# Optimization experiments

Measured on AMD Instinct MI355X. Metric: run time of the kernel, lower is better.

The kernel has to match this reference:

```python
import jax, jax.numpy as jnp
import numpy as np

D_MODEL = 256
N_HEADS = 8
HEAD_DIM = D_MODEL // N_HEADS


def setup_inputs() -> dict:
    key = jax.random.key(0)
    ks = jax.random.split(key, 10)
    B, L, D = 2, 2048, D_MODEL
    s = 1.0 / np.sqrt(D)
    inp = {
        "x": jax.random.normal(ks[0], (B, L, D), dtype=jnp.float32),
        "Wq": jax.random.normal(ks[1], (D, D), dtype=jnp.float32) * s,
        "bq": jnp.zeros((D,), jnp.float32),
        "Wk": jax.random.normal(ks[2], (D, D), dtype=jnp.float32) * s,
        "bk": jnp.zeros((D,), jnp.float32),
        "Wv": jax.random.normal(ks[3], (D, D), dtype=jnp.float32) * s,
        "bv": jnp.zeros((D,), jnp.float32),
        "u": jax.random.normal(ks[4], (N_HEADS, 1, 1), dtype=jnp.float32) * 0.1,
        "Wo": jax.random.normal(ks[5], (D, D), dtype=jnp.float32) * s,
        "bo": jnp.zeros((D,), jnp.float32),
    }
    return inp


def reference(x, Wq, bq, Wk, bk, Wv, bv, u, Wo, bo):
    B, L, D = x.shape
    H, hd = N_HEADS, HEAD_DIM

    def proj(W, b):  # torch Linear: x @ W.T + b -> [B,H,L,hd]
        return (x @ W.T + b).reshape(B, L, H, hd).transpose(0, 2, 1, 3)

    Q, K, V = proj(Wq, bq), proj(Wk, bk), proj(Wv, bv)

    scores = jnp.einsum("bhqd,bhkd->bhqk", Q, K) / np.sqrt(hd)
    attn_series = jax.nn.softmax(scores, axis=-1)  # [B,H,L,L]

    pos = jnp.arange(L, dtype=jnp.float32)
    dist = jnp.abs(pos[None, :] - pos[:, None])  # [L,L]
    # prior per head: exp(-d^2 / (2*(u^2+1e-6))), normalized over last dim
    prior = jnp.exp(-(dist[None] ** 2) / (2.0 * (u ** 2 + 1e-6)))  # [H,L,L]
    prior = prior / (prior.sum(axis=-1, keepdims=True) + 1e-6)

    discrepancy = jnp.abs(attn_series - prior[None]).mean(axis=(1, 2))  # [B,L]

    out = jnp.einsum("bhqk,bhkd->bhqd", attn_series, V)
    out = out.transpose(0, 2, 1, 3).reshape(B, L, D)
    out = out @ Wo.T + bo
    return out, discrepancy
```

## Files before the change

### kernel.cpp

```cpp
#include <hip/hip_runtime.h>
#include <hip/hip_bf16.h>
#include <math.h>

#define LSEQ 2048
#define DMODEL 256
#define NH 8
#define HD 32

typedef __attribute__((ext_vector_type(8))) short bf16x8;
typedef __attribute__((ext_vector_type(4))) float f32x4;

#define MFMA __builtin_amdgcn_mfma_f32_16x16x32_bf16

__device__ __forceinline__ short f2bf(float x) {
  __hip_bfloat16 h = __float2bfloat16(x);
  return __builtin_bit_cast(short, h);
}
__device__ __forceinline__ float bf2f(short s) {
  __hip_bfloat16 h = __builtin_bit_cast(__hip_bfloat16, s);
  return __bfloat162float(h);
}
__device__ __forceinline__ short bftrunc(float x) {
  return (short)(__builtin_bit_cast(unsigned int, x) >> 16);
}
__device__ __forceinline__ float fexp2(float x) {
#if __has_builtin(__builtin_amdgcn_exp2f)
  return __builtin_amdgcn_exp2f(x);
#else
  return __expf(x * 0.6931471805599453f);
#endif
}
__device__ __forceinline__ float flog2(float x) {
#if __has_builtin(__builtin_amdgcn_logf)
  return __builtin_amdgcn_logf(x);
#else
  return __logf(x) * 1.4426950408889634f;
#endif
}

__global__ __launch_bounds__(256) void aux_kernel(
    const float* __restrict__ Wq, const float* __restrict__ Wk,
    const float* __restrict__ Wv, const float* __restrict__ Wo,
    const float* __restrict__ u,
    short* __restrict__ Wh,
    short* __restrict__ Woh, short* __restrict__ Wol,
    float* __restrict__ Eb, float* __restrict__ Zb)
{
  __shared__ float Cs[LSEQ];
  __shared__ float part[256];
  const int tid = threadIdx.x;
  if (blockIdx.x < 256) {
    const int i4 = (blockIdx.x * 256 + tid) * 4;
    if (i4 < 196608) {
      int row = i4 >> 8, col = i4 & 255;
      const float* W = (row < 256) ? Wq : (row < 512) ? Wk : Wv;
      float4 v = *(const float4*)(W + (row & 255) * 256 + col);
      *(short4*)(Wh + i4) = make_short4(f2bf(v.x), f2bf(v.y), f2bf(v.z), f2bf(v.w));
    } else {
      int j = i4 - 196608;
      float4 v = *(const float4*)(Wo + j);
      short h0 = f2bf(v.x), h1 = f2bf(v.y), h2 = f2bf(v.z), h3 = f2bf(v.w);
      *(short4*)(Woh + j) = make_short4(h0, h1, h2, h3);
      *(short4*)(Wol + j) = make_short4(bftrunc(v.x - bf2f(h0)), bftrunc(v.y - bf2f(h1)),
                                        bftrunc(v.z - bf2f(h2)), bftrunc(v.w - bf2f(h3)));
    }
    return;
  }
  const int h = blockIdx.x - 256;
  const float uu = u[h];
  const float den = 2.0f * (uu * uu + 1e-6f);
  float e[8]; float run = 0.f;
  const int base = tid * 8;
#pragma unroll
  for (int j = 0; j < 8; ++j) {
    float d = (float)(base + j);
    e[j] = __expf(-(d * d) / den);
    run += e[j];
  }
  part[tid] = run;
  __syncthreads();
  for (int off = 1; off < 256; off <<= 1) {
    float v = (tid >= off) ? part[tid - off] : 0.f;
    __syncthreads();
    part[tid] += v;
    __syncthreads();
  }
  float c = part[tid] - run;
#pragma unroll
  for (int j = 0; j < 8; ++j) {
    c += e[j];
    Cs[base + j] = c;
    Eb[h * LSEQ + base + j] = e[j];
  }
  __syncthreads();
  const float E0 = Cs[0];
  for (int i = tid; i < LSEQ; i += 256) {
    float s = Cs[i] + Cs[LSEQ - 1 - i] - E0;
    Zb[h * LSEQ + i] = 1.0f / (s + 1e-6f);
  }
}

__global__ __launch_bounds__(256) void qkv_gemm(
    const float* __restrict__ x,
    const short* __restrict__ Bh,
    const float* __restrict__ bq, const float* __restrict__ bk,
    const float* __restrict__ bv,
    short* __restrict__ Qf, short* __restrict__ Kf, short* __restrict__ Vf)
{
  const int tid = threadIdx.x, w = tid >> 6, lane = tid & 63;
  const int l15 = lane & 15, q4 = lane >> 4;
  const int m0 = blockIdx.x * 64, n0 = blockIdx.y * 64;
  const int mrow = m0 + w * 16 + l15;
  f32x4 acc[4] = {{0,0,0,0},{0,0,0,0},{0,0,0,0},{0,0,0,0}};
  for (int k0 = 0; k0 < 256; k0 += 32) {
    const float* xp = &x[(size_t)mrow * 256 + k0 + q4 * 8];
    float4 a = *(const float4*)xp;
    float4 c = *(const float4*)(xp + 4);
    bf16x8 ah;
    ah[0] = f2bf(a.x); ah[1] = f2bf(a.y); ah[2] = f2bf(a.z); ah[3] = f2bf(a.w);
    ah[4] = f2bf(c.x); ah[5] = f2bf(c.y); ah[6] = f2bf(c.z); ah[7] = f2bf(c.w);
#pragma unroll
    for (int nt = 0; nt < 4; ++nt) {
      const size_t bi = (size_t)(n0 + nt * 16 + l15) * 256 + k0 + q4 * 8;
      bf16x8 bh = *(const bf16x8*)&Bh[bi];
      acc[nt] = MFMA(ah, bh, acc[nt], 0, 0, 0);
    }
  }
  const int type = n0 >> 8;
  const int n0l = n0 & 255;
  const float* bias = (type == 0) ? bq : (type == 1) ? bk : bv;
  const float qls = 0.25503489f;
#pragma unroll
  for (int nt = 0; nt < 4; ++nt) {
    const int col = n0l + nt * 16 + l15;
    const float bvv = bias[col];
    const int hh = col >> 5, dloc = col & 31;
#pragma unroll
    for (int r = 0; r < 4; ++r) {
      const int m = m0 + w * 16 + q4 * 4 + r;
      float v = acc[nt][r] + bvv;
      const int bb = m >> 11, mm = m & 2047, rr = mm & 15;
      if (type == 2) {
        const int kt128 = mm >> 7, low7 = mm & 127;
        const int wv = (low7 >> 4) & 3, ph = low7 >> 6;
        const int c = ph * 16 + rr;
        const size_t idx =
          ((((((size_t)bb * 8 + hh) * 16 + kt128) * 4 + wv) * 2 + (dloc >> 4)) * 64
           + (c >> 3) * 16 + (dloc & 15)) * 8 + (c & 7);
        Vf[idx] = f2bf(v);
      } else if (type == 0) {
        const int qblk = mm >> 5, rg = (mm >> 4) & 1;
        const size_t idx =
          (((((size_t)bb * 8 + hh) * 64 + qblk) * 2 + rg) * 64
           + (dloc >> 3) * 16 + rr) * 8 + (dloc & 7);
        Qf[idx] = f2bf(v * qls);
      } else {
        const int g = mm >> 4;
        const size_t idx =
          ((((size_t)bb * 8 + hh) * 128 + g) * 64
           + (dloc >> 3) * 16 + rr) * 8 + (dloc & 7);
        Kf[idx] = f2bf(v);
      }
    }
  }
}

__global__ __launch_bounds__(256) void out_gemm(
    const short* __restrict__ Ah, const short* __restrict__ Al,
    const short* __restrict__ Bh, const short* __restrict__ Bl,
    const float* __restrict__ bias, float* __restrict__ C)
{
  const int tid = threadIdx.x, w = tid >> 6, lane = tid & 63;
  const int l15 = lane & 15, q4 = lane >> 4;
  const int m0 = blockIdx.x * 64, n0 = blockIdx.y * 64;
  const int mrow = m0 + w * 16 + l15;
  f32x4 acc[4] = {{0,0,0,0},{0,0,0,0},{0,0,0,0},{0,0,0,0}};
  for (int k0 = 0; k0 < 256; k0 += 32) {
    bf16x8 ah = *(const bf16x8*)&Ah[(size_t)mrow * 256 + k0 + q4 * 8];
    bf16x8 al = *(const bf16x8*)&Al[(size_t)mrow * 256 + k0 + q4 * 8];
#pragma unroll
    for (int nt = 0; nt < 4; ++nt) {
      const size_t bi = (size_t)(n0 + nt * 16 + l15) * 256 + k0 + q4 * 8;
      bf16x8 bh = *(const bf16x8*)&Bh[bi];
      bf16x8 bl = *(const bf16x8*)&Bl[bi];
      acc[nt] = MFMA(ah, bh, acc[nt], 0, 0, 0);
      acc[nt] = MFMA(al, bh, acc[nt], 0, 0, 0);
      acc[nt] = MFMA(ah, bl, acc[nt], 0, 0, 0);
    }
  }
#pragma unroll
  for (int nt = 0; nt < 4; ++nt) {
    const int col = n0 + nt * 16 + l15;
    const float bvv = bias[col];
#pragma unroll
    for (int r = 0; r < 4; ++r) {
      const int m = m0 + w * 16 + q4 * 4 + r;
      C[(size_t)m * 256 + col] = acc[nt][r] + bvv;
    }
  }
}

__global__ __launch_bounds__(256, 8) void attn_kernel(
    const short* __restrict__ Qf, const short* __restrict__ Kf,
    const short* __restrict__ Vf,
    const float* __restrict__ Eb, const float* __restrict__ Zb,
    short* __restrict__ Ohb, short* __restrict__ Olb,
    short* __restrict__ Dp)
{
  __shared__ short Pt[4][16][40];
  __shared__ float Elds[192];
  __shared__ float lpart[4][16];
  __shared__ float izlds[16];

  const int tid = threadIdx.x, w = tid >> 6, lane = tid & 63;
  const int l15 = lane & 15, q4 = lane >> 4;
  const int flat = blockIdx.x + 128 * (blockIdx.y + 8 * blockIdx.z);
  const int slot = flat >> 3;
  const int g = (flat & 7) | ((slot >> 7) << 3);
  const int h = g & 7, b = g >> 3;
  const int qslot = slot & 127, q0 = qslot * 16;
  const int bh = b * NH + h;

  if (tid < 192) Elds[tid] = Eb[h * LSEQ + tid];
  if (tid < 16)  izlds[tid] = Zb[h * LSEQ + q0 + tid];

  const bf16x8* Qf8 = (const bf16x8*)Qf;
  const bf16x8* Kf8 = (const bf16x8*)Kf;
  const bf16x8* Vf8 = (const bf16x8*)Vf;

  bf16x8 qh = Qf8[((size_t)bh * 128 + qslot) * 64 + lane];
  __syncthreads();

  const size_t kfb = (size_t)bh * 128;
  const size_t vfb = (size_t)bh * 16;

  float lac[4] = {0.f, 0.f, 0.f, 0.f};
#pragma unroll 2
  for (int kt = 0; kt < LSEQ; kt += 128) {
    bf16x8 k0 = Kf8[(kfb + (kt >> 4) + w) * 64 + lane];
    bf16x8 k1 = Kf8[(kfb + (kt >> 4) + 4 + w) * 64 + lane];
    f32x4 s0 = {0.f, 0.f, 0.f, 0.f};
    s0 = MFMA(qh, k0, s0, 0, 0, 0);
    f32x4 s1 = {0.f, 0.f, 0.f, 0.f};
    s1 = MFMA(qh, k1, s1, 0, 0, 0);
#pragma unroll
    for (int r = 0; r < 4; ++r) lac[r] += fexp2(s0[r]) + fexp2(s1[r]);
  }
#pragma unroll
  for (int r = 0; r < 4; ++r) {
    float v = lac[r];
    v += __shfl_xor(v, 1); v += __shfl_xor(v, 2);
    v += __shfl_xor(v, 4); v += __shfl_xor(v, 8);
    lac[r] = v;
  }
  if (l15 == 0) {
#pragma unroll
    for (int r = 0; r < 4; ++r) lpart[w][q4 * 4 + r] = lac[r];
  }
  __syncthreads();
  f32x4 sinit;
#pragma unroll
  for (int r = 0; r < 4; ++r) {
    const int qi = q4 * 4 + r;
    sinit[r] = -flog2(lpart[0][qi] + lpart[1][qi] + lpart[2][qi] + lpart[3][qi]);
  }

  const size_t drow = (size_t)(g * 128 + qslot) * LSEQ;
  f32x4 oacc[2] = {{0,0,0,0},{0,0,0,0}};
#pragma unroll 2
  for (int kt = 0; kt < LSEQ; kt += 128) {
    bf16x8 kh0 = Kf8[(kfb + (kt >> 4) + w) * 64 + lane];
    bf16x8 kh1 = Kf8[(kfb + (kt >> 4) + 4 + w) * 64 + lane];
    bf16x8 vb0 = Vf8[(((vfb + (kt >> 7)) * 4 + w) * 2 + 0) * 64 + lane];
    bf16x8 vb1 = Vf8[(((vfb + (kt >> 7)) * 4 + w) * 2 + 1) * 64 + lane];
#pragma unroll
    for (int ph = 0; ph < 2; ++ph) {
      bf16x8 kbh = ph ? kh1 : kh0;
      const int c0 = kt + ph * 64 + w * 16;
      const int kg = c0 + l15;
      const int dd = c0 - q0;
      const bool near = (dd >= -96) && (dd <= 96);
      float dsum = 0.f;
      f32x4 s = sinit;
      s = MFMA(qh, kbh, s, 0, 0, 0);
#pragma unroll
      for (int r = 0; r < 4; ++r) {
        float p = fexp2(s[r]);
        Pt[w][q4 * 4 + r][ph * 16 + l15] = bftrunc(p);
        if (near) {
          int qrow = q0 + q4 * 4 + r;
          int dist = (qrow >= kg) ? (qrow - kg) : (kg - qrow);
          dsum += fabsf(p - Elds[dist] * izlds[q4 * 4 + r]);
        } else {
          dsum += p;
        }
      }
      dsum += __shfl_xor(dsum, 16);
      dsum += __shfl_xor(dsum, 32);
      if (q4 == 0) Dp[drow + kg] = f2bf(dsum);
    }
    bf16x8 pa = *(const bf16x8*)&Pt[w][l15][q4 * 8];
    oacc[0] = MFMA(pa, vb0, oacc[0], 0, 0, 0);
    oacc[1] = MFMA(pa, vb1, oacc[1], 0, 0, 0);
  }

  __syncthreads();
  float* Ored = (float*)&Pt[0][0][0];
#pragma unroll
  for (int dt = 0; dt < 2; ++dt) {
#pragma unroll
    for (int r = 0; r < 4; ++r)
      Ored[(w * 16 + q4 * 4 + r) * 17 + l15] = oacc[dt][r];
    __syncthreads();
    {
      const int q = tid >> 4, d = tid & 15;
      float v = Ored[q * 17 + d] + Ored[(16 + q) * 17 + d] +
                Ored[(32 + q) * 17 + d] + Ored[(48 + q) * 17 + d];
      const size_t oo = ((size_t)b * LSEQ + q0 + q) * DMODEL + h * HD + dt * 16 + d;
      short hi = f2bf(v);
      Ohb[oo] = hi;
      Olb[oo] = bftrunc(v - bf2f(hi));
    }
    __syncthreads();
  }
}

__global__ __launch_bounds__(256) void disc_reduce(
    const short* __restrict__ Dp, float* __restrict__ disc)
{
  __shared__ float red[8][33];
  const int tid = threadIdx.x;
  const int b = blockIdx.x >> 6;
  const int kb = (blockIdx.x & 63) * 32;
  const int k = kb + (tid & 31), sg = tid >> 5;
  float acc = 0.f;
  const short* base = Dp + ((size_t)b * 1024 + (size_t)sg * 128) * LSEQ + k;
#pragma unroll 4
  for (int i = 0; i < 128; ++i) acc += bf2f(base[(size_t)i * LSEQ]);
  red[sg][tid & 31] = acc;
  __syncthreads();
  if (tid < 32) {
    float v = 0.f;
#pragma unroll
    for (int s2 = 0; s2 < 8; ++s2) v += red[s2][tid];
    disc[b * LSEQ + kb + tid] = v * (1.0f / ((float)NH * (float)LSEQ));
  }
}

extern "C" void kernel_launch(void* const* d_in, const int* in_sizes, int n_in,
                              void* d_out, int out_size, void* d_ws, size_t ws_size,
                              hipStream_t stream)
{
  const float* x  = (const float*)d_in[0];
  const float* Wq = (const float*)d_in[1];
  const float* bq = (const float*)d_in[2];
  const float* Wk = (const float*)d_in[3];
  const float* bk = (const float*)d_in[4];
  const float* Wv = (const float*)d_in[5];
  const float* bv = (const float*)d_in[6];
  const float* u  = (const float*)d_in[7];
  const float* Wo = (const float*)d_in[8];
  const float* bo = (const float*)d_in[9];

  float* out  = (float*)d_out;
  float* disc = out + (size_t)2 * LSEQ * DMODEL;

  char* w8 = (char*)d_ws;
  const size_t MB = 1u << 20;
  short* Qfb = (short*)(w8);
  short* Kfb = (short*)(w8 + 2 * MB);
  short* Vfb = (short*)(w8 + 4 * MB);
  short* Ohb = (short*)(w8 + 6 * MB);
  short* Olb = (short*)(w8 + 8 * MB);
  short* Wh  = (short*)(w8 + 10 * MB);
  short* Woh = (short*)(w8 + 10 * MB + 393216);
  short* Wol = (short*)(w8 + 10 * MB + 524288);
  float* Eb  = (float*)(w8 + 11 * MB);
  float* Zb  = (float*)(w8 + 11 * MB + 65536);
  short* Dp  = (short*)(w8 + 12 * MB);

  aux_kernel<<<264, 256, 0, stream>>>(Wq, Wk, Wv, Wo, u, Wh, Woh, Wol, Eb, Zb);
  qkv_gemm<<<dim3(64, 12), 256, 0, stream>>>(x, Wh, bq, bk, bv, Qfb, Kfb, Vfb);
  attn_kernel<<<dim3(128, 8, 2), 256, 0, stream>>>(Qfb, Kfb, Vfb, Eb, Zb,
                                                   Ohb, Olb, Dp);
  disc_reduce<<<128, 256, 0, stream>>>(Dp, disc);
  out_gemm<<<dim3(64, 4), 256, 0, stream>>>(Ohb, Olb, Woh, Wol, bo, out);
}
```

Measured before the change: 156.7 us.

## Process two query tiles per attention block, pre-convert x, narrow out_gemm tiles

The attention kernel now handles 32 query rows per block as two 16-row tiles that share each loaded K and V fragment. This halves the global K/V traffic and the block count, and the discrepancy partial rows are halved to match in disc_reduce. Separately, x is converted to bf16 once in the aux kernel so qkv_gemm loads bf16 directly instead of converting per block. out_gemm uses 32-wide N tiles to double its grid. In exchange, attention uses more registers and shared memory, occupancy is lowered to 4 blocks, and there is a larger serialized epilogue with four reduction passes.

```diff
diff --git a/kernel.cpp b/kernel.cpp
--- a/kernel.cpp
+++ b/kernel.cpp
@@ -39,9 +39,11 @@
 }
 
 __global__ __launch_bounds__(256) void aux_kernel(
+    const float* __restrict__ x,
     const float* __restrict__ Wq, const float* __restrict__ Wk,
     const float* __restrict__ Wv, const float* __restrict__ Wo,
     const float* __restrict__ u,
+    short* __restrict__ xh,
     short* __restrict__ Wh,
     short* __restrict__ Woh, short* __restrict__ Wol,
     float* __restrict__ Eb, float* __restrict__ Zb)
@@ -49,8 +51,15 @@
   __shared__ float Cs[LSEQ];
   __shared__ float part[256];
   const int tid = threadIdx.x;
-  if (blockIdx.x < 256) {
+  if (blockIdx.x < 1024) {
     const int i4 = (blockIdx.x * 256 + tid) * 4;
+    float4 v = *(const float4*)(x + i4);
+    *(short4*)(xh + i4) = make_short4(f2bf(v.x), f2bf(v.y), f2bf(v.z), f2bf(v.w));
+    return;
+  }
+  const int bx = blockIdx.x - 1024;
+  if (bx < 256) {
+    const int i4 = (bx * 256 + tid) * 4;
     if (i4 < 196608) {
       int row = i4 >> 8, col = i4 & 255;
       const float* W = (row < 256) ? Wq : (row < 512) ? Wk : Wv;
@@ -66,7 +75,7 @@
     }
     return;
   }
-  const int h = blockIdx.x - 256;
+  const int h = bx - 256;
   const float uu = u[h];
   const float den = 2.0f * (uu * uu + 1e-6f);
   float e[8]; float run = 0.f;
@@ -101,7 +110,7 @@
 }
 
 __global__ __launch_bounds__(256) void qkv_gemm(
-    const float* __restrict__ x,
+    const short* __restrict__ xh,
     const short* __restrict__ Bh,
     const float* __restrict__ bq, const float* __restrict__ bk,
     const float* __restrict__ bv,
@@ -113,12 +122,7 @@
   const int mrow = m0 + w * 16 + l15;
   f32x4 acc[4] = {{0,0,0,0},{0,0,0,0},{0,0,0,0},{0,0,0,0}};
   for (int k0 = 0; k0 < 256; k0 += 32) {
-    const float* xp = &x[(size_t)mrow * 256 + k0 + q4 * 8];
-    float4 a = *(const float4*)xp;
-    float4 c = *(const float4*)(xp + 4);
-    bf16x8 ah;
-    ah[0] = f2bf(a.x); ah[1] = f2bf(a.y); ah[2] = f2bf(a.z); ah[3] = f2bf(a.w);
-    ah[4] = f2bf(c.x); ah[5] = f2bf(c.y); ah[6] = f2bf(c.z); ah[7] = f2bf(c.w);
+    bf16x8 ah = *(const bf16x8*)&xh[(size_t)mrow * 256 + k0 + q4 * 8];
 #pragma unroll
     for (int nt = 0; nt < 4; ++nt) {
       const size_t bi = (size_t)(n0 + nt * 16 + l15) * 256 + k0 + q4 * 8;
@@ -172,14 +176,14 @@
 {
   const int tid = threadIdx.x, w = tid >> 6, lane = tid & 63;
   const int l15 = lane & 15, q4 = lane >> 4;
-  const int m0 = blockIdx.x * 64, n0 = blockIdx.y * 64;
+  const int m0 = blockIdx.x * 64, n0 = blockIdx.y * 32;
   const int mrow = m0 + w * 16 + l15;
-  f32x4 acc[4] = {{0,0,0,0},{0,0,0,0},{0,0,0,0},{0,0,0,0}};
+  f32x4 acc[2] = {{0,0,0,0},{0,0,0,0}};
   for (int k0 = 0; k0 < 256; k0 += 32) {
     bf16x8 ah = *(const bf16x8*)&Ah[(size_t)mrow * 256 + k0 + q4 * 8];
     bf16x8 al = *(const bf16x8*)&Al[(size_t)mrow * 256 + k0 + q4 * 8];
 #pragma unroll
-    for (int nt = 0; nt < 4; ++nt) {
+    for (int nt = 0; nt < 2; ++nt) {
       const size_t bi = (size_t)(n0 + nt * 16 + l15) * 256 + k0 + q4 * 8;
       bf16x8 bh = *(const bf16x8*)&Bh[bi];
       bf16x8 bl = *(const bf16x8*)&Bl[bi];
@@ -189,7 +193,7 @@
     }
   }
 #pragma unroll
-  for (int nt = 0; nt < 4; ++nt) {
+  for (int nt = 0; nt < 2; ++nt) {
     const int col = n0 + nt * 16 + l15;
     const float bvv = bias[col];
 #pragma unroll
@@ -200,73 +204,86 @@
   }
 }
 
-__global__ __launch_bounds__(256, 8) void attn_kernel(
+__global__ __launch_bounds__(256, 4) void attn_kernel(
     const short* __restrict__ Qf, const short* __restrict__ Kf,
     const short* __restrict__ Vf,
     const float* __restrict__ Eb, const float* __restrict__ Zb,
     short* __restrict__ Ohb, short* __restrict__ Olb,
     short* __restrict__ Dp)
 {
-  __shared__ short Pt[4][16][40];
+  __shared__ short Pt[2][4][16][40];
   __shared__ float Elds[192];
-  __shared__ float lpart[4][16];
-  __shared__ float izlds[16];
+  __shared__ float lpart[2][4][16];
+  __shared__ float izlds[32];
 
   const int tid = threadIdx.x, w = tid >> 6, lane = tid & 63;
   const int l15 = lane & 15, q4 = lane >> 4;
-  const int flat = blockIdx.x + 128 * (blockIdx.y + 8 * blockIdx.z);
+  const int flat = blockIdx.x + 64 * (blockIdx.y + 8 * blockIdx.z);
   const int slot = flat >> 3;
-  const int g = (flat & 7) | ((slot >> 7) << 3);
+  const int g = (flat & 7) | ((slot >> 6) << 3);
   const int h = g & 7, b = g >> 3;
-  const int qslot = slot & 127, q0 = qslot * 16;
+  const int qpair = slot & 63;
+  const int q0 = qpair * 32;
   const int bh = b * NH + h;
 
   if (tid < 192) Elds[tid] = Eb[h * LSEQ + tid];
-  if (tid < 16)  izlds[tid] = Zb[h * LSEQ + q0 + tid];
+  if (tid < 32)  izlds[tid] = Zb[h * LSEQ + q0 + tid];
 
   const bf16x8* Qf8 = (const bf16x8*)Qf;
   const bf16x8* Kf8 = (const bf16x8*)Kf;
   const bf16x8* Vf8 = (const bf16x8*)Vf;
 
-  bf16x8 qh = Qf8[((size_t)bh * 128 + qslot) * 64 + lane];
+  bf16x8 qhA = Qf8[((size_t)bh * 128 + qpair * 2 + 0) * 64 + lane];
+  bf16x8 qhB = Qf8[((size_t)bh * 128 + qpair * 2 + 1) * 64 + lane];
   __syncthreads();
 
   const size_t kfb = (size_t)bh * 128;
   const size_t vfb = (size_t)bh * 16;
 
-  float lac[4] = {0.f, 0.f, 0.f, 0.f};
+  float lacA[4] = {0.f, 0.f, 0.f, 0.f};
+  float lacB[4] = {0.f, 0.f, 0.f, 0.f};
 #pragma unroll 2
   for (int kt = 0; kt < LSEQ; kt += 128) {
     bf16x8 k0 = Kf8[(kfb + (kt >> 4) + w) * 64 + lane];
     bf16x8 k1 = Kf8[(kfb + (kt >> 4) + 4 + w) * 64 + lane];
-    f32x4 s0 = {0.f, 0.f, 0.f, 0.f};
-    s0 = MFMA(qh, k0, s0, 0, 0, 0);
-    f32x4 s1 = {0.f, 0.f, 0.f, 0.f};
-    s1 = MFMA(qh, k1, s1, 0, 0, 0);
-#pragma unroll
-    for (int r = 0; r < 4; ++r) lac[r] += fexp2(s0[r]) + fexp2(s1[r]);
+    f32x4 sA0 = {0.f,0.f,0.f,0.f}; sA0 = MFMA(qhA, k0, sA0, 0, 0, 0);
+    f32x4 sB0 = {0.f,0.f,0.f,0.f}; sB0 = MFMA(qhB, k0, sB0, 0, 0, 0);
+    f32x4 sA1 = {0.f,0.f,0.f,0.f}; sA1 = MFMA(qhA, k1, sA1, 0, 0, 0);
+    f32x4 sB1 = {0.f,0.f,0.f,0.f}; sB1 = MFMA(qhB, k1, sB1, 0, 0, 0);
+#pragma unroll
+    for (int r = 0; r < 4; ++r) {
+      lacA[r] += fexp2(sA0[r]) + fexp2(sA1[r]);
+      lacB[r] += fexp2(sB0[r]) + fexp2(sB1[r]);
+    }
   }
 #pragma unroll
   for (int r = 0; r < 4; ++r) {
-    float v = lac[r];
-    v += __shfl_xor(v, 1); v += __shfl_xor(v, 2);
-    v += __shfl_xor(v, 4); v += __shfl_xor(v, 8);
-    lac[r] = v;
+    float a = lacA[r], bb2 = lacB[r];
+    a += __shfl_xor(a, 1); a += __shfl_xor(a, 2);
+    a += __shfl_xor(a, 4); a += __shfl_xor(a, 8);
+    bb2 += __shfl_xor(bb2, 1); bb2 += __shfl_xor(bb2, 2);
+    bb2 += __shfl_xor(bb2, 4); bb2 += __shfl_xor(bb2, 8);
+    lacA[r] = a; lacB[r] = bb2;
   }
   if (l15 == 0) {
 #pragma unroll
-    for (int r = 0; r < 4; ++r) lpart[w][q4 * 4 + r] = lac[r];
-  }
-  __syncthreads();
-  f32x4 sinit;
+    for (int r = 0; r < 4; ++r) {
+      lpart[0][w][q4 * 4 + r] = lacA[r];
+      lpart[1][w][q4 * 4 + r] = lacB[r];
+    }
+  }
+  __syncthreads();
+  f32x4 sinitA, sinitB;
 #pragma unroll
   for (int r = 0; r < 4; ++r) {
     const int qi = q4 * 4 + r;
-    sinit[r] = -flog2(lpart[0][qi] + lpart[1][qi] + lpart[2][qi] + lpart[3][qi]);
-  }
-
-  const size_t drow = (size_t)(g * 128 + qslot) * LSEQ;
-  f32x4 oacc[2] = {{0,0,0,0},{0,0,0,0}};
+    sinitA[r] = -flog2(lpart[0][0][qi] + lpart[0][1][qi] + lpart[0][2][qi] + lpart[0][3][qi]);
+    sinitB[r] = -flog2(lpart[1][0][qi] + lpart[1][1][qi] + lpart[1][2][qi] + lpart[1][3][qi]);
+  }
+
+  const size_t drow = (size_t)(g * 64 + qpair) * LSEQ;
+  f32x4 oaccA[2] = {{0,0,0,0},{0,0,0,0}};
+  f32x4 oaccB[2] = {{0,0,0,0},{0,0,0,0}};
 #pragma unroll 2
   for (int kt = 0; kt < LSEQ; kt += 128) {
     bf16x8 kh0 = Kf8[(kfb + (kt >> 4) + w) * 64 + lane];
@@ -278,51 +295,71 @@
       bf16x8 kbh = ph ? kh1 : kh0;
       const int c0 = kt + ph * 64 + w * 16;
       const int kg = c0 + l15;
-      const int dd = c0 - q0;
-      const bool near = (dd >= -96) && (dd <= 96);
+      const int ddA = c0 - q0;
+      const int ddB = ddA - 16;
+      const bool nearA = (ddA >= -96) && (ddA <= 96);
+      const bool nearB = (ddB >= -96) && (ddB <= 96);
+      f32x4 sA = sinitA; sA = MFMA(qhA, kbh, sA, 0, 0, 0);
+      f32x4 sB = sinitB; sB = MFMA(qhB, kbh, sB, 0, 0, 0);
       float dsum = 0.f;
-      f32x4 s = sinit;
-      s = MFMA(qh, kbh, s, 0, 0, 0);
 #pragma unroll
       for (int r = 0; r < 4; ++r) {
-        float p = fexp2(s[r]);
-        Pt[w][q4 * 4 + r][ph * 16 + l15] = bftrunc(p);
-        if (near) {
+        float pA = fexp2(sA[r]);
+        Pt[0][w][q4 * 4 + r][ph * 16 + l15] = bftrunc(pA);
+        if (nearA) {
           int qrow = q0 + q4 * 4 + r;
           int dist = (qrow >= kg) ? (qrow - kg) : (kg - qrow);
-          dsum += fabsf(p - Elds[dist] * izlds[q4 * 4 + r]);
+          dsum += fabsf(pA - Elds[dist] * izlds[q4 * 4 + r]);
         } else {
-          dsum += p;
+          dsum += pA;
+        }
+      }
+#pragma unroll
+      for (int r = 0; r < 4; ++r) {
+        float pB = fexp2(sB[r]);
+        Pt[1][w][q4 * 4 + r][ph * 16 + l15] = bftrunc(pB);
+        if (nearB) {
+          int qrow = q0 + 16 + q4 * 4 + r;
+          int dist = (qrow >= kg) ? (qrow - kg) : (kg - qrow);
+          dsum += fabsf(pB - Elds[dist] * izlds[16 + q4 * 4 + r]);
+        } else {
+          dsum += pB;
         }
       }
       dsum += __shfl_xor(dsum, 16);
       dsum += __shfl_xor(dsum, 32);
       if (q4 == 0) Dp[drow + kg] = f2bf(dsum);
     }
-    bf16x8 pa = *(const bf16x8*)&Pt[w][l15][q4 * 8];
-    oacc[0] = MFMA(pa, vb0, oacc[0], 0, 0, 0);
-    oacc[1] = MFMA(pa, vb1, oacc[1], 0, 0, 0);
-  }
-
-  __syncthreads();
-  float* Ored = (float*)&Pt[0][0][0];
-#pragma unroll
-  for (int dt = 0; dt < 2; ++dt) {
+    bf16x8 paA = *(const bf16x8*)&Pt[0][w][l15][q4 * 8];
+    bf16x8 paB = *(const bf16x8*)&Pt[1][w][l15][q4 * 8];
+    oaccA[0] = MFMA(paA, vb0, oaccA[0], 0, 0, 0);
+    oaccB[0] = MFMA(paB, vb0, oaccB[0], 0, 0, 0);
+    oaccA[1] = MFMA(paA, vb1, oaccA[1], 0, 0, 0);
+    oaccB[1] = MFMA(paB, vb1, oaccB[1], 0, 0, 0);
+  }
+
+  __syncthreads();
+  float* Ored = (float*)&Pt[0][0][0][0];
+  auto store_tile = [&](f32x4 o, int trow, int dt) {
 #pragma unroll
     for (int r = 0; r < 4; ++r)
-      Ored[(w * 16 + q4 * 4 + r) * 17 + l15] = oacc[dt][r];
+      Ored[(w * 16 + q4 * 4 + r) * 17 + l15] = o[r];
     __syncthreads();
     {
       const int q = tid >> 4, d = tid & 15;
       float v = Ored[q * 17 + d] + Ored[(16 + q) * 17 + d] +
                 Ored[(32 + q) * 17 + d] + Ored[(48 + q) * 17 + d];
-      const size_t oo = ((size_t)b * LSEQ + q0 + q) * DMODEL + h * HD + dt * 16 + d;
+      const size_t oo = ((size_t)b * LSEQ + q0 + trow + q) * DMODEL + h * HD + dt * 16 + d;
       short hi = f2bf(v);
       Ohb[oo] = hi;
       Olb[oo] = bftrunc(v - bf2f(hi));
     }
     __syncthreads();
-  }
+  };
+  store_tile(oaccA[0], 0, 0);
+  store_tile(oaccA[1], 0, 1);
+  store_tile(oaccB[0], 16, 0);
+  store_tile(oaccB[1], 16, 1);
 }
 
 __global__ __launch_bounds__(256) void disc_reduce(
@@ -334,9 +371,9 @@
   const int kb = (blockIdx.x & 63) * 32;
   const int k = kb + (tid & 31), sg = tid >> 5;
   float acc = 0.f;
-  const short* base = Dp + ((size_t)b * 1024 + (size_t)sg * 128) * LSEQ + k;
+  const short* base = Dp + ((size_t)b * 512 + (size_t)sg * 64) * LSEQ + k;
 #pragma unroll 4
-  for (int i = 0; i < 128; ++i) acc += bf2f(base[(size_t)i * LSEQ]);
+  for (int i = 0; i < 64; ++i) acc += bf2f(base[(size_t)i * LSEQ]);
   red[sg][tid & 31] = acc;
   __syncthreads();
   if (tid < 32) {
@@ -377,12 +414,13 @@
   short* Wol = (short*)(w8 + 10 * MB + 524288);
   float* Eb  = (float*)(w8 + 11 * MB);
   float* Zb  = (float*)(w8 + 11 * MB + 65536);
-  short* Dp  = (short*)(w8 + 12 * MB);
-
-  aux_kernel<<<264, 256, 0, stream>>>(Wq, Wk, Wv, Wo, u, Wh, Woh, Wol, Eb, Zb);
-  qkv_gemm<<<dim3(64, 12), 256, 0, stream>>>(x, Wh, bq, bk, bv, Qfb, Kfb, Vfb);
-  attn_kernel<<<dim3(128, 8, 2), 256, 0, stream>>>(Qfb, Kfb, Vfb, Eb, Zb,
-                                                   Ohb, Olb, Dp);
+  short* xh  = (short*)(w8 + 12 * MB);
+  short* Dp  = (short*)(w8 + 14 * MB);
+
+  aux_kernel<<<1288, 256, 0, stream>>>(x, Wq, Wk, Wv, Wo, u, xh, Wh, Woh, Wol, Eb, Zb);
+  qkv_gemm<<<dim3(64, 12), 256, 0, stream>>>(xh, Wh, bq, bk, bv, Qfb, Kfb, Vfb);
+  attn_kernel<<<dim3(64, 8, 2), 256, 0, stream>>>(Qfb, Kfb, Vfb, Eb, Zb,
+                                                  Ohb, Olb, Dp);
   disc_reduce<<<128, 256, 0, stream>>>(Dp, disc);
-  out_gemm<<<dim3(64, 4), 256, 0, stream>>>(Ohb, Olb, Woh, Wol, bo, out);
-}
+  out_gemm<<<dim3(64, 8), 256, 0, stream>>>(Ohb, Olb, Woh, Wol, bo, out);
+}
```

Result: faster. 147.6 us (-5.8%).
